# Optimization experiments

Hardware: AMD Instinct MI355X
Metric: run time of the kernel (lower is better)

## Reference

```python
import math
import jax, jax.numpy as jnp
import numpy as np

B, C, E = 8, 2048, 1024

def setup_inputs() -> dict:
    key = jax.random.key(0)
    ks = jax.random.split(key, 7)
    s_e = 1.0 / math.sqrt(E)
    s_c = 1.0 / math.sqrt(C)
    return {
        'x': jax.random.normal(ks[0], (B, C, E), dtype=jnp.float32),
        'fc_w': jax.random.normal(ks[1], (E, E), dtype=jnp.float32) * s_e,
        'fc_b': jax.random.normal(ks[2], (E,), dtype=jnp.float32) * s_e,
        'alt_fc_w': jax.random.normal(ks[3], (C, C), dtype=jnp.float32) * s_c,
        'alt_fc_b': jax.random.normal(ks[4], (C,), dtype=jnp.float32) * s_c,
        'vfc_w': jax.random.normal(ks[5], (E, E), dtype=jnp.float32) * s_e,
        'vfc_b': jax.random.normal(ks[6], (E,), dtype=jnp.float32) * s_e,
    }

def reference(x, fc_w, fc_b, alt_fc_w, alt_fc_b, vfc_w, vfc_b):
    # y = fc(x): [b,c,e]
    y = jnp.einsum('bce,fe->bcf', x, fc_w) + fc_b
    # yx = alt_fc(x^T): [b,e,c] -> Linear over context dim -> [b,e,k]
    xx = jnp.swapaxes(x, 1, 2)                    # [b,e,c]
    yx = jnp.einsum('bec,kc->bek', xx, alt_fc_w) + alt_fc_b
    # attention scores: [b,c,k]
    attn = jnp.einsum('bce,bek->bck', y, yx)
    scale = 1.0 / math.sqrt(attn.shape[-1])
    attn = jax.nn.softmax(attn * scale, axis=-1)
    # values
    vx = jnp.einsum('bke,fe->bkf', x, vfc_w) + vfc_b
    out = jnp.einsum('bck,bke->bce', attn, vx)
    # post_feed=None -> return y only
    return out
```

## Files before the change

### kernel.cpp

```cpp
#include <hip/hip_runtime.h>
#include <stdint.h>

#define Bb 8
#define Cc 2048
#define Ee 1024

typedef unsigned short u16;
typedef __attribute__((ext_vector_type(8))) short short8;
typedef __attribute__((ext_vector_type(4))) float f32x4;

__device__ __forceinline__ u16 f2bf(float f){
    unsigned u = __builtin_bit_cast(unsigned, f);
    return (u16)((u + 0x7fffu + ((u >> 16) & 1u)) >> 16);
}
__device__ __forceinline__ float bf2f(u16 h){
    return __builtin_bit_cast(float, ((unsigned)h) << 16);
}
__device__ __forceinline__ void gld16(const void* g, void* l){
    __builtin_amdgcn_global_load_lds(
        (const __attribute__((address_space(1))) unsigned int*)g,
        (__attribute__((address_space(3))) unsigned int*)l,
        16, 0, 0);
}
#define MFMA(a,b,c) __builtin_amdgcn_mfma_f32_16x16x32_bf16((a),(b),(c),0,0,0)
#define SBAR()  __builtin_amdgcn_s_barrier()
#define SCHED0() __builtin_amdgcn_sched_barrier(0)
#define LGKM8() asm volatile("s_waitcnt lgkmcnt(8)" ::: "memory")
#define LGKM4() asm volatile("s_waitcnt lgkmcnt(4)" ::: "memory")
#define LGKM0() asm volatile("s_waitcnt lgkmcnt(0)" ::: "memory")
#define VMCNT0() asm volatile("s_waitcnt vmcnt(0)" ::: "memory")

__global__ __launch_bounds__(256) void k_cast(const float* __restrict__ s,
                                              u16* __restrict__ d, long n4){
    long i = (long)blockIdx.x * 256 + threadIdx.x;
    const long stride = (long)gridDim.x * 256;
    for (; i < n4; i += stride){
        float4 f = ((const float4*)s)[i];
        ushort4 o = make_ushort4(f2bf(f.x), f2bf(f.y), f2bf(f.z), f2bf(f.w));
        ((ushort4*)d)[i] = o;
    }
}

__global__ __launch_bounds__(256) void k_cast_xt(const float* __restrict__ src,
                                                 u16* __restrict__ xb,
                                                 u16* __restrict__ xbT){
    __shared__ float tile[32][33];
    const int b = blockIdx.z;
    src += (long)b * Cc * Ee;
    xb  += (long)b * Cc * Ee;
    xbT += (long)b * Cc * Ee;
    const int c0 = blockIdx.x * 32;
    const int r0 = blockIdx.y * 32;
    const int tx = threadIdx.x & 31;
    const int ty = threadIdx.x >> 5;
    #pragma unroll
    for (int p = 0; p < 4; ++p){
        float v = src[(long)(r0 + ty + p*8) * Ee + c0 + tx];
        tile[ty + p*8][tx] = v;
        xb[(long)(r0 + ty + p*8) * Ee + c0 + tx] = f2bf(v);
    }
    __syncthreads();
    #pragma unroll
    for (int p = 0; p < 4; ++p)
        xbT[(long)(c0 + ty + p*8) * Cc + r0 + tx] = f2bf(tile[tx][ty + p*8]);
}

template<int BIAS_MODE, int OUT_F32>
__global__ __launch_bounds__(512, 2)
void k_gemm256(const u16* __restrict__ A, const u16* __restrict__ Bm,
               void* __restrict__ Cout, const float* __restrict__ bias,
               int N, int K, long sA, long sB, long sC, float scale)
{
    __shared__ __attribute__((aligned(16))) char smem[131072];

    const int gx = gridDim.x, gy = gridDim.y;
    const int nwg = gx * gy * gridDim.z;
    const int lin = blockIdx.x + gx * (blockIdx.y + gy * blockIdx.z);
    const int swz = (lin & 7) * (nwg >> 3) + (lin >> 3);
    const int bx = swz % gx;
    const int tmp = swz / gx;
    const int by = tmp % gy;
    const int bz = tmp / gy;

    A  += (long)bz * sA;
    Bm += (long)bz * sB;
    u16*   Cm = (u16*)Cout + (OUT_F32 ? 0 : (long)bz * sC);
    float* Cf = (float*)Cout + (OUT_F32 ? (long)bz * sC : 0);

    const int tid  = threadIdx.x;
    const int lane = tid & 63;
    const int wave = tid >> 6;
    const int wr = wave >> 2;
    const int wc = wave & 3;
    const int tileM = bx * 256;
    const int tileN = by * 256;

    const int srow   = tid >> 3;
    const int schunk = (tid & 7) ^ (srow & 7);
    const u16* Ag = A  + (long)(tileM + srow) * K + schunk * 8;
    const u16* Bg = Bm + (long)(tileN + srow) * K + schunk * 8;
    const long uK = (long)64 * K;
    const int  ldst = tid * 16;

    const int lrow = lane & 15;
    const int lk   = lane >> 4;
    const int sw   = lrow & 7;
    const int cs0  = ((0 + lk) ^ sw) * 16;
    const int cs1  = ((4 + lk) ^ sw) * 16;
    const int arow0 = (wr*128 + lrow) * 128;
    const int brow0 = 32768 + (wc*64 + lrow) * 128;

    f32x4 acc[8][4];
    #pragma unroll
    for (int m = 0; m < 8; ++m)
        #pragma unroll
        for (int n = 0; n < 4; ++n)
            acc[m][n] = (f32x4){0.f,0.f,0.f,0.f};

    char* sm = smem;
    #pragma unroll
    for (int u = 0; u < 4; ++u) gld16(Bg + u*uK, sm + 32768 + u*8192 + ldst);
    #pragma unroll
    for (int u = 0; u < 4; ++u) gld16(Ag + u*uK, sm + u*8192 + ldst);
    __syncthreads();

    const int NT = K >> 6;
    short8 aE[4], aO[4], bE[4], bO[4];

    for (int t = 0; t < NT; ++t){
        const bool pref = (t + 1) < NT;
        char* cbuf = sm + ((t & 1) << 16);
        char* nbuf = sm + (((t + 1) & 1) << 16);
        const u16* Agt = Ag + (long)(t + 1) * 64;
        const u16* Bgt = Bg + (long)(t + 1) * 64;

        if (pref){
            gld16(Agt + 0*uK, nbuf + 0*8192 + ldst);
            gld16(Agt + 1*uK, nbuf + 1*8192 + ldst);
            gld16(Agt + 2*uK, nbuf + 2*8192 + ldst);
            gld16(Agt + 3*uK, nbuf + 3*8192 + ldst);
            gld16(Bgt + 0*uK, nbuf + 32768 + 0*8192 + ldst);
            gld16(Bgt + 1*uK, nbuf + 32768 + 1*8192 + ldst);
            gld16(Bgt + 2*uK, nbuf + 32768 + 2*8192 + ldst);
            gld16(Bgt + 3*uK, nbuf + 32768 + 3*8192 + ldst);
        }

        #pragma unroll
        for (int m = 0; m < 4; ++m) aE[m] = *(const short8*)(cbuf + arow0 + m*2048 + cs0);
        #pragma unroll
        for (int n = 0; n < 4; ++n) bE[n] = *(const short8*)(cbuf + brow0 + n*2048 + cs0);
        #pragma unroll
        for (int m = 0; m < 4; ++m) aO[m] = *(const short8*)(cbuf + arow0 + (m+4)*2048 + cs0);

        LGKM4(); SCHED0();
        __builtin_amdgcn_s_setprio(1);
        #pragma unroll
        for (int m = 0; m < 4; ++m)
            #pragma unroll
            for (int n = 0; n < 4; ++n)
                acc[m][n] = MFMA(aE[m], bE[n], acc[m][n]);
        __builtin_amdgcn_s_setprio(0);

        #pragma unroll
        for (int m = 0; m < 4; ++m) aE[m] = *(const short8*)(cbuf + arow0 + m*2048 + cs1);
        #pragma unroll
        for (int n = 0; n < 4; ++n) bO[n] = *(const short8*)(cbuf + brow0 + n*2048 + cs1);
        LGKM8(); SCHED0();
        __builtin_amdgcn_s_setprio(1);
        #pragma unroll
        for (int m = 0; m < 4; ++m)
            #pragma unroll
            for (int n = 0; n < 4; ++n)
                acc[m+4][n] = MFMA(aO[m], bE[n], acc[m+4][n]);
        __builtin_amdgcn_s_setprio(0);

        #pragma unroll
        for (int m = 0; m < 4; ++m) aO[m] = *(const short8*)(cbuf + arow0 + (m+4)*2048 + cs1);
        LGKM4(); SCHED0();
        __builtin_amdgcn_s_setprio(1);
        #pragma unroll
        for (int m = 0; m < 4; ++m)
            #pragma unroll
            for (int n = 0; n < 4; ++n)
                acc[m][n] = MFMA(aE[m], bO[n], acc[m][n]);
        __builtin_amdgcn_s_setprio(0);

        LGKM0(); SCHED0();
        __builtin_amdgcn_s_setprio(1);
        #pragma unroll
        for (int m = 0; m < 4; ++m)
            #pragma unroll
            for (int n = 0; n < 4; ++n)
                acc[m+4][n] = MFMA(aO[m], bO[n], acc[m+4][n]);
        __builtin_amdgcn_s_setprio(0);

        VMCNT0(); SBAR(); SCHED0();
    }

    const int r0base = tileM + wr*128 + lk*4;
    const int cbase  = tileN + wc*64 + lrow;
    #pragma unroll
    for (int m = 0; m < 8; ++m){
        const int r0 = r0base + m*16;
        #pragma unroll
        for (int n = 0; n < 4; ++n){
            const int c = cbase + n*16;
            f32x4 v = acc[m][n];
            #pragma unroll
            for (int j = 0; j < 4; ++j){
                float val = v[j] * scale;
                if (BIAS_MODE == 1) val += bias[c];
                if (BIAS_MODE == 2) val += bias[r0 + j];
                if (OUT_F32) Cf[(long)(r0 + j) * N + c] = val;
                else         Cm[(long)(r0 + j) * N + c] = f2bf(val);
            }
        }
    }
}

__global__ __launch_bounds__(256) void k_softmax(u16* __restrict__ P){
    u16* p = P + (long)blockIdx.x * Cc;
    const int tid = threadIdx.x;
    short8 raw = *(const short8*)(p + tid * 8);
    float v[8];
    float mx = -3.0e38f;
    #pragma unroll
    for (int i = 0; i < 8; ++i){ v[i] = bf2f((u16)raw[i]); mx = fmaxf(mx, v[i]); }
    #pragma unroll
    for (int o = 32; o > 0; o >>= 1) mx = fmaxf(mx, __shfl_xor(mx, o));
    __shared__ float redm[4];
    if ((tid & 63) == 0) redm[tid >> 6] = mx;
    __syncthreads();
    mx = fmaxf(fmaxf(redm[0], redm[1]), fmaxf(redm[2], redm[3]));
    float s = 0.f;
    #pragma unroll
    for (int i = 0; i < 8; ++i){ v[i] = __expf(v[i] - mx); s += v[i]; }
    #pragma unroll
    for (int o = 32; o > 0; o >>= 1) s += __shfl_xor(s, o);
    __shared__ float reds[4];
    if ((tid & 63) == 0) reds[tid >> 6] = s;
    __syncthreads();
    s = reds[0] + reds[1] + reds[2] + reds[3];
    const float inv = 1.f / s;
    short8 o8;
    #pragma unroll
    for (int i = 0; i < 8; ++i) o8[i] = (short)f2bf(v[i] * inv);
    *(short8*)(p + tid * 8) = o8;
}

static inline int cast_grid(long n4){
    long g = (n4 + 255) / 256;
    return (int)(g > 2048 ? 2048 : g);
}

extern "C" void kernel_launch(void* const* d_in, const int* in_sizes, int n_in,
                              void* d_out, int out_size, void* d_ws, size_t ws_size,
                              hipStream_t stream)
{
    const float* x     = (const float*)d_in[0];
    const float* fc_w  = (const float*)d_in[1];
    const float* fc_b  = (const float*)d_in[2];
    const float* altw  = (const float*)d_in[3];
    const float* altb  = (const float*)d_in[4];
    const float* vfc_w = (const float*)d_in[5];
    const float* vfc_b = (const float*)d_in[6];
    float* out = (float*)d_out;

    char* ws = (char*)d_ws;
    const size_t nBCE = (size_t)Bb * Cc * Ee;
    u16* xb   = (u16*)(ws);
    u16* xbT  = (u16*)(ws + 2 * nBCE);
    u16* P    = (u16*)(ws);
    u16* y    = (u16*)(ws + 4 * nBCE);
    u16* z    = (u16*)(ws + 6 * nBCE);
    u16* vxT  = (u16*)(ws + 8 * nBCE);
    u16* fcwb = (u16*)(ws + 10 * nBCE);
    u16* vfwb = fcwb + (size_t)Ee * Ee;
    u16* awb  = vfwb + (size_t)Ee * Ee;

    k_cast_xt<<<dim3(Ee / 32, Cc / 32, Bb), 256, 0, stream>>>(x, xb, xbT);
    k_cast<<<cast_grid((long)Ee * Ee / 4), 256, 0, stream>>>(fc_w, fcwb, (long)Ee * Ee / 4);
    k_cast<<<cast_grid((long)Ee * Ee / 4), 256, 0, stream>>>(vfc_w, vfwb, (long)Ee * Ee / 4);
    k_cast<<<cast_grid((long)Cc * Cc / 4), 256, 0, stream>>>(altw, awb, (long)Cc * Cc / 4);

    const long sBCE = (long)Cc * Ee;
    const long sBCC = (long)Cc * Cc;
    dim3 blk(512);

    k_gemm256<1, 0><<<dim3(Cc/256, Ee/256, Bb), blk, 0, stream>>>(
        xb, fcwb, y, fc_b, Ee, Ee, sBCE, 0, sBCE, 1.f);

    k_gemm256<2, 0><<<dim3(Ee/256, Cc/256, Bb), blk, 0, stream>>>(
        vfwb, xb, vxT, vfc_b, Cc, Ee, 0, sBCE, sBCE, 1.f);

    k_gemm256<2, 0><<<dim3(Cc/256, Ee/256, Bb), blk, 0, stream>>>(
        awb, xbT, z, altb, Ee, Cc, 0, sBCE, sBCE, 1.f);

    k_gemm256<0, 0><<<dim3(Cc/256, Cc/256, Bb), blk, 0, stream>>>(
        y, z, P, nullptr, Cc, Ee, sBCE, sBCE, sBCC, 0.022097086912079608f);

    k_softmax<<<Bb * Cc, 256, 0, stream>>>(P);

    k_gemm256<0, 1><<<dim3(Cc/256, Ee/256, Bb), blk, 0, stream>>>(
        P, vxT, out, nullptr, Ee, Cc, sBCC, sBCE, sBCE, 1.f);
}
```

Before: 339.3 us.

## Fuse softmax into score GEMM epilogue and normalize in output GEMM

```diff
diff --git a/kernel.cpp b/kernel.cpp
--- a/kernel.cpp
+++ b/kernel.cpp
@@ -29,17 +29,6 @@
 #define LGKM4() asm volatile("s_waitcnt lgkmcnt(4)" ::: "memory")
 #define LGKM0() asm volatile("s_waitcnt lgkmcnt(0)" ::: "memory")
 #define VMCNT0() asm volatile("s_waitcnt vmcnt(0)" ::: "memory")
-
-__global__ __launch_bounds__(256) void k_cast(const float* __restrict__ s,
-                                              u16* __restrict__ d, long n4){
-    long i = (long)blockIdx.x * 256 + threadIdx.x;
-    const long stride = (long)gridDim.x * 256;
-    for (; i < n4; i += stride){
-        float4 f = ((const float4*)s)[i];
-        ushort4 o = make_ushort4(f2bf(f.x), f2bf(f.y), f2bf(f.z), f2bf(f.w));
-        ((ushort4*)d)[i] = o;
-    }
-}
 
 __global__ __launch_bounds__(256) void k_cast_xt(const float* __restrict__ src,
                                                  u16* __restrict__ xb,
@@ -65,10 +54,27 @@
         xbT[(long)(c0 + ty + p*8) * Cc + r0 + tx] = f2bf(tile[tx][ty + p*8]);
 }
 
-template<int BIAS_MODE, int OUT_F32>
+__global__ __launch_bounds__(256) void k_cast3(const float* __restrict__ s0, u16* __restrict__ d0, long n0,
+                                               const float* __restrict__ s1, u16* __restrict__ d1, long n1,
+                                               const float* __restrict__ s2, u16* __restrict__ d2, long n2){
+    long i = (long)blockIdx.x * 256 + threadIdx.x;
+    const long stride = (long)gridDim.x * 256;
+    const long tot = n0 + n1 + n2;
+    for (; i < tot; i += stride){
+        const float* s; u16* d; long k;
+        if (i < n0)          { s = s0; d = d0; k = i; }
+        else if (i < n0 + n1){ s = s1; d = d1; k = i - n0; }
+        else                 { s = s2; d = d2; k = i - n0 - n1; }
+        float4 f = ((const float4*)s)[k];
+        ((ushort4*)d)[k] = make_ushort4(f2bf(f.x), f2bf(f.y), f2bf(f.z), f2bf(f.w));
+    }
+}
+
+template<int BIAS_MODE, int OUT_F32, int EPI, int PRIO>
 __global__ __launch_bounds__(512, 2)
 void k_gemm256(const u16* __restrict__ A, const u16* __restrict__ Bm,
                void* __restrict__ Cout, const float* __restrict__ bias,
+               float* __restrict__ extra,
                int N, int K, long sA, long sB, long sC, float scale)
 {
     __shared__ __attribute__((aligned(16))) char smem[131072];
@@ -153,104 +159,115 @@
         for (int m = 0; m < 4; ++m) aO[m] = *(const short8*)(cbuf + arow0 + (m+4)*2048 + cs0);
 
         LGKM4(); SCHED0();
-        __builtin_amdgcn_s_setprio(1);
+        if (PRIO) __builtin_amdgcn_s_setprio(1);
         #pragma unroll
         for (int m = 0; m < 4; ++m)
             #pragma unroll
             for (int n = 0; n < 4; ++n)
                 acc[m][n] = MFMA(aE[m], bE[n], acc[m][n]);
-        __builtin_amdgcn_s_setprio(0);
+        if (PRIO) __builtin_amdgcn_s_setprio(0);
 
         #pragma unroll
         for (int m = 0; m < 4; ++m) aE[m] = *(const short8*)(cbuf + arow0 + m*2048 + cs1);
         #pragma unroll
         for (int n = 0; n < 4; ++n) bO[n] = *(const short8*)(cbuf + brow0 + n*2048 + cs1);
         LGKM8(); SCHED0();
-        __builtin_amdgcn_s_setprio(1);
+        if (PRIO) __builtin_amdgcn_s_setprio(1);
         #pragma unroll
         for (int m = 0; m < 4; ++m)
             #pragma unroll
             for (int n = 0; n < 4; ++n)
                 acc[m+4][n] = MFMA(aO[m], bE[n], acc[m+4][n]);
-        __builtin_amdgcn_s_setprio(0);
+        if (PRIO) __builtin_amdgcn_s_setprio(0);
 
         #pragma unroll
         for (int m = 0; m < 4; ++m) aO[m] = *(const short8*)(cbuf + arow0 + (m+4)*2048 + cs1);
         LGKM4(); SCHED0();
-        __builtin_amdgcn_s_setprio(1);
+        if (PRIO) __builtin_amdgcn_s_setprio(1);
         #pragma unroll
         for (int m = 0; m < 4; ++m)
             #pragma unroll
             for (int n = 0; n < 4; ++n)
                 acc[m][n] = MFMA(aE[m], bO[n], acc[m][n]);
-        __builtin_amdgcn_s_setprio(0);
+        if (PRIO) __builtin_amdgcn_s_setprio(0);
 
         LGKM0(); SCHED0();
-        __builtin_amdgcn_s_setprio(1);
+        if (PRIO) __builtin_amdgcn_s_setprio(1);
         #pragma unroll
         for (int m = 0; m < 4; ++m)
             #pragma unroll
             for (int n = 0; n < 4; ++n)
                 acc[m+4][n] = MFMA(aO[m], bO[n], acc[m+4][n]);
-        __builtin_amdgcn_s_setprio(0);
+        if (PRIO) __builtin_amdgcn_s_setprio(0);
 
         VMCNT0(); SBAR(); SCHED0();
     }
 
     const int r0base = tileM + wr*128 + lk*4;
     const int cbase  = tileN + wc*64 + lrow;
-    #pragma unroll
-    for (int m = 0; m < 8; ++m){
-        const int r0 = r0base + m*16;
-        #pragma unroll
-        for (int n = 0; n < 4; ++n){
-            const int c = cbase + n*16;
-            f32x4 v = acc[m][n];
+
+    if (EPI == 0){
+        #pragma unroll
+        for (int m = 0; m < 8; ++m){
+            const int r0 = r0base + m*16;
+            #pragma unroll
+            for (int n = 0; n < 4; ++n){
+                const int c = cbase + n*16;
+                f32x4 v = acc[m][n];
+                #pragma unroll
+                for (int j = 0; j < 4; ++j){
+                    float val = v[j] * scale;
+                    if (BIAS_MODE == 1) val += bias[c];
+                    if (BIAS_MODE == 2) val += bias[r0 + j];
+                    if (OUT_F32) Cf[(long)(r0 + j) * N + c] = val;
+                    else         Cm[(long)(r0 + j) * N + c] = f2bf(val);
+                }
+            }
+        }
+    } else if (EPI == 1){
+        float* lsum = (float*)smem;
+        const int rl0 = wr*128 + lk*4;
+        #pragma unroll
+        for (int m = 0; m < 8; ++m){
+            const int r0 = r0base + m*16;
             #pragma unroll
             for (int j = 0; j < 4; ++j){
-                float val = v[j] * scale;
-                if (BIAS_MODE == 1) val += bias[c];
-                if (BIAS_MODE == 2) val += bias[r0 + j];
-                if (OUT_F32) Cf[(long)(r0 + j) * N + c] = val;
-                else         Cm[(long)(r0 + j) * N + c] = f2bf(val);
+                float rp = 0.f;
+                #pragma unroll
+                for (int n = 0; n < 4; ++n){
+                    float e = __expf(acc[m][n][j] * scale);
+                    rp += e;
+                    Cm[(long)(r0 + j) * N + (cbase + n*16)] = f2bf(e);
+                }
+                rp += __shfl_xor(rp, 1);
+                rp += __shfl_xor(rp, 2);
+                rp += __shfl_xor(rp, 4);
+                rp += __shfl_xor(rp, 8);
+                if (lrow == 0)
+                    lsum[(rl0 + m*16 + j)*4 + wc] = rp;
             }
         }
+        __syncthreads();
+        if (tid < 256){
+            float4 v4 = ((const float4*)lsum)[tid];
+            extra[((long)bz*Cc + tileM + tid)*8 + by] = v4.x + v4.y + v4.z + v4.w;
+        }
+    } else {
+        #pragma unroll
+        for (int m = 0; m < 8; ++m){
+            const int r0 = r0base + m*16;
+            #pragma unroll
+            for (int j = 0; j < 4; ++j){
+                const float4* pr = (const float4*)(extra + ((long)bz*Cc + r0 + j)*8);
+                float4 pa = pr[0], pb = pr[1];
+                float S = pa.x+pa.y+pa.z+pa.w + pb.x+pb.y+pb.z+pb.w;
+                const float inv = 1.f / S;
+                #pragma unroll
+                for (int n = 0; n < 4; ++n)
+                    Cf[(long)(r0 + j) * N + (cbase + n*16)] = acc[m][n][j] * inv;
+            }
+        }
     }
-}
-
-__global__ __launch_bounds__(256) void k_softmax(u16* __restrict__ P){
-    u16* p = P + (long)blockIdx.x * Cc;
-    const int tid = threadIdx.x;
-    short8 raw = *(const short8*)(p + tid * 8);
-    float v[8];
-    float mx = -3.0e38f;
-    #pragma unroll
-    for (int i = 0; i < 8; ++i){ v[i] = bf2f((u16)raw[i]); mx = fmaxf(mx, v[i]); }
-    #pragma unroll
-    for (int o = 32; o > 0; o >>= 1) mx = fmaxf(mx, __shfl_xor(mx, o));
-    __shared__ float redm[4];
-    if ((tid & 63) == 0) redm[tid >> 6] = mx;
-    __syncthreads();
-    mx = fmaxf(fmaxf(redm[0], redm[1]), fmaxf(redm[2], redm[3]));
-    float s = 0.f;
-    #pragma unroll
-    for (int i = 0; i < 8; ++i){ v[i] = __expf(v[i] - mx); s += v[i]; }
-    #pragma unroll
-    for (int o = 32; o > 0; o >>= 1) s += __shfl_xor(s, o);
-    __shared__ float reds[4];
-    if ((tid & 63) == 0) reds[tid >> 6] = s;
-    __syncthreads();
-    s = reds[0] + reds[1] + reds[2] + reds[3];
-    const float inv = 1.f / s;
-    short8 o8;
-    #pragma unroll
-    for (int i = 0; i < 8; ++i) o8[i] = (short)f2bf(v[i] * inv);
-    *(short8*)(p + tid * 8) = o8;
-}
-
-static inline int cast_grid(long n4){
-    long g = (n4 + 255) / 256;
-    return (int)(g > 2048 ? 2048 : g);
 }
 
 extern "C" void kernel_launch(void* const* d_in, const int* in_sizes, int n_in,
@@ -277,30 +294,29 @@
     u16* fcwb = (u16*)(ws + 10 * nBCE);
     u16* vfwb = fcwb + (size_t)Ee * Ee;
     u16* awb  = vfwb + (size_t)Ee * Ee;
+    float* rpart = (float*)(ws + 10 * nBCE);
 
     k_cast_xt<<<dim3(Ee / 32, Cc / 32, Bb), 256, 0, stream>>>(x, xb, xbT);
-    k_cast<<<cast_grid((long)Ee * Ee / 4), 256, 0, stream>>>(fc_w, fcwb, (long)Ee * Ee / 4);
-    k_cast<<<cast_grid((long)Ee * Ee / 4), 256, 0, stream>>>(vfc_w, vfwb, (long)Ee * Ee / 4);
-    k_cast<<<cast_grid((long)Cc * Cc / 4), 256, 0, stream>>>(altw, awb, (long)Cc * Cc / 4);
+    k_cast3<<<2048, 256, 0, stream>>>(fc_w, fcwb, (long)Ee * Ee / 4,
+                                      vfc_w, vfwb, (long)Ee * Ee / 4,
+                                      altw, awb, (long)Cc * Cc / 4);
 
     const long sBCE = (long)Cc * Ee;
     const long sBCC = (long)Cc * Cc;
     dim3 blk(512);
 
-    k_gemm256<1, 0><<<dim3(Cc/256, Ee/256, Bb), blk, 0, stream>>>(
-        xb, fcwb, y, fc_b, Ee, Ee, sBCE, 0, sBCE, 1.f);
-
-    k_gemm256<2, 0><<<dim3(Ee/256, Cc/256, Bb), blk, 0, stream>>>(
-        vfwb, xb, vxT, vfc_b, Cc, Ee, 0, sBCE, sBCE, 1.f);
-
-    k_gemm256<2, 0><<<dim3(Cc/256, Ee/256, Bb), blk, 0, stream>>>(
-        awb, xbT, z, altb, Ee, Cc, 0, sBCE, sBCE, 1.f);
-
-    k_gemm256<0, 0><<<dim3(Cc/256, Cc/256, Bb), blk, 0, stream>>>(
-        y, z, P, nullptr, Cc, Ee, sBCE, sBCE, sBCC, 0.022097086912079608f);
-
-    k_softmax<<<Bb * Cc, 256, 0, stream>>>(P);
-
-    k_gemm256<0, 1><<<dim3(Cc/256, Ee/256, Bb), blk, 0, stream>>>(
-        P, vxT, out, nullptr, Ee, Cc, sBCC, sBCE, sBCE, 1.f);
-}
+    k_gemm256<1, 0, 0, 1><<<dim3(Cc/256, Ee/256, Bb), blk, 0, stream>>>(
+        xb, fcwb, y, fc_b, nullptr, Ee, Ee, sBCE, 0, sBCE, 1.f);
+
+    k_gemm256<2, 0, 0, 1><<<dim3(Ee/256, Cc/256, Bb), blk, 0, stream>>>(
+        vfwb, xb, vxT, vfc_b, nullptr, Cc, Ee, 0, sBCE, sBCE, 1.f);
+
+    k_gemm256<2, 0, 0, 0><<<dim3(Cc/256, Ee/256, Bb), blk, 0, stream>>>(
+        awb, xbT, z, altb, nullptr, Ee, Cc, 0, sBCE, sBCE, 1.f);
+
+    k_gemm256<0, 0, 1, 1><<<dim3(Cc/256, Cc/256, Bb), blk, 0, stream>>>(
+        y, z, P, nullptr, rpart, Cc, Ee, sBCE, sBCE, sBCC, 0.022097086912079608f);
+
+    k_gemm256<0, 1, 2, 0><<<dim3(Cc/256, Ee/256, Bb), blk, 0, stream>>>(
+        P, vxT, out, nullptr, rpart, Ee, Cc, sBCC, sBCE, sBCE, 1.f);
+}
```

After: 309.1 us. 1.1x faster.
